# Performance work log

Measured on AMD Instinct MI355X. Metric: run time of the kernel, lower is better.

## Reference

```python
import jax, jax.numpy as jnp
import numpy as np
from jax import lax

V = 50257   # dict_len (vocab)
E = 1024    # w2v_size
H = 1024    # hidden_dim
S = 512     # source length
NSTEPS = 128


def _lstm_cell(h, c, x, W_ih, W_hh, b_ih, b_hh):
    # torch LSTM gate order: i, f, g, o ; W_ih: [4H, in], W_hh: [4H, H]
    gates = x @ W_ih.T + h @ W_hh.T + b_ih + b_hh  # [4H]
    i, f, g, o = jnp.split(gates, 4)
    i = jax.nn.sigmoid(i)
    f = jax.nn.sigmoid(f)
    g = jnp.tanh(g)
    o = jax.nn.sigmoid(o)
    c = f * c + i * g
    h = o * jnp.tanh(c)
    return h, c


def setup_inputs() -> dict:
    key = jax.random.key(0)
    ks = jax.random.split(key, 14)
    s = 0.02
    f32 = jnp.float32
    return {
        "source": jax.random.randint(ks[0], (S,), 0, V),
        "n_steps": NSTEPS,
        "start_token": 1,
        "Wemb_enc": jax.random.normal(ks[1], (V, E), f32) * s,
        "W_ih_e": jax.random.normal(ks[2], (4 * H, E), f32) * s,
        "W_hh_e": jax.random.normal(ks[3], (4 * H, H), f32) * s,
        "b_ih_e": jnp.zeros((4 * H,), f32),
        "b_hh_e": jnp.zeros((4 * H,), f32),
        "Wemb_dec": jax.random.normal(ks[4], (V, E), f32) * s,
        "W_ih_d": jax.random.normal(ks[5], (4 * H, E), f32) * s,
        "W_hh_d": jax.random.normal(ks[6], (4 * H, H), f32) * s,
        "b_ih_d": jnp.zeros((4 * H,), f32),
        "b_hh_d": jnp.zeros((4 * H,), f32),
        "W_out": jax.random.normal(ks[7], (V, H), f32) * s,
        "b_out": jnp.zeros((V,), f32),
    }


def reference(source, n_steps, start_token,
              Wemb_enc, W_ih_e, W_hh_e, b_ih_e, b_hh_e,
              Wemb_dec, W_ih_d, W_hh_d, b_ih_d, b_hh_d,
              W_out, b_out):
    dt = Wemb_enc.dtype

    # ---- encoder: run LSTM over embedded source, keep final (h, c) ----
    xs = Wemb_enc[source]  # [S, E]

    def enc_step(carry, x):
        h, c = carry
        h, c = _lstm_cell(h, c, x, W_ih_e, W_hh_e, b_ih_e, b_hh_e)
        return (h, c), None

    h0 = jnp.zeros((H,), dt)
    c0 = jnp.zeros((H,), dt)
    (h, c), _ = lax.scan(enc_step, (h0, c0), xs)

    def dec_step(carry, _):
        h, c, tok = carry
        x = Wemb_dec[tok]  # [E]
        h, c = _lstm_cell(h, c, x, W_ih_d, W_hh_d, b_ih_d, b_hh_d)
        logits = h @ W_out.T + b_out        # [V]
        probs = jax.nn.softmax(logits)       # module applies Softmax then argmax
        tok = jnp.argmax(probs).astype(jnp.int32)
        return (h, c, tok), (tok, probs)

    tok0 = jnp.asarray(start_token, jnp.int32)
    _, (tokens, probs) = lax.scan(dec_step, (h, c, tok0), None, length=int(n_steps))
    return tokens, probs  # [n_steps] int32, [n_steps, V]
```

## Files before the change

### kernel.cpp

```cpp
#include <hip/hip_runtime.h>
#include <math.h>

#define HDIM  1024
#define VDIM  50257
#define NBLK  256
#define NTHR  1024
#define NWAVE 16

typedef unsigned int uint;

#define WS_GATES   0
#define WS_PSOFT   32768
#define WS_PARGV   33792
#define WS_PARGI   34816
#define WS_PSUM    35840
#define WS_ARRIVE  36864
#define WS_DONE    69632
#define WS_ZOFF    32768
#define WS_ZLEN    40960
#define WS_W8      131072
#define W8_BYTES   ((size_t)VDIM * HDIM)

#if __has_builtin(__builtin_amdgcn_cvt_pk_f32_fp8) && __has_builtin(__builtin_amdgcn_cvt_pk_fp8_f32)
#define FP8_HW 1
#else
#define FP8_HW 0
#endif

__device__ __forceinline__ float dot4(float4 a, float4 b) {
  return a.x * b.x + a.y * b.y + a.z * b.z + a.w * b.w;
}

#if !FP8_HW
__device__ __forceinline__ float fp8d(uint b) {
  uint em = b & 0x7fu;
  float m;
  if (em >= 8u) m = __uint_as_float(((((em >> 3) + 120u) << 23) | ((em & 7u) << 20)));
  else          m = (float)em * 0.001953125f;
  return (b & 0x80u) ? -m : m;
}
__device__ __forceinline__ uint fp8e(float x) {
  uint s = (__float_as_uint(x) >> 24) & 0x80u;
  float ax = fabsf(x);
  uint r;
  if (ax < 0.015625f) {
    r = (uint)rintf(ax * 512.f);
  } else {
    uint b = __float_as_uint(ax);
    b += 0x7ffffu + ((b >> 20) & 1u);
    int  e8 = (int)(b >> 23) - 127 + 7;
    uint m8 = (b >> 20) & 7u;
    if (e8 >= 16 || (e8 == 15 && m8 == 7u)) { e8 = 15; m8 = 6u; }
    r = ((uint)e8 << 3) | m8;
  }
  return r | s;
}
#endif

__device__ __forceinline__ float dot16_fp8(uint4 u, float4 h0, float4 h1,
                                           float4 h2, float4 h3) {
#if FP8_HW
  float s = 0.f;
  { auto a = __builtin_amdgcn_cvt_pk_f32_fp8((int)u.x, false);
    auto b = __builtin_amdgcn_cvt_pk_f32_fp8((int)u.x, true);
    s += a[0] * h0.x + a[1] * h0.y + b[0] * h0.z + b[1] * h0.w; }
  { auto a = __builtin_amdgcn_cvt_pk_f32_fp8((int)u.y, false);
    auto b = __builtin_amdgcn_cvt_pk_f32_fp8((int)u.y, true);
    s += a[0] * h1.x + a[1] * h1.y + b[0] * h1.z + b[1] * h1.w; }
  { auto a = __builtin_amdgcn_cvt_pk_f32_fp8((int)u.z, false);
    auto b = __builtin_amdgcn_cvt_pk_f32_fp8((int)u.z, true);
    s += a[0] * h2.x + a[1] * h2.y + b[0] * h2.z + b[1] * h2.w; }
  { auto a = __builtin_amdgcn_cvt_pk_f32_fp8((int)u.w, false);
    auto b = __builtin_amdgcn_cvt_pk_f32_fp8((int)u.w, true);
    s += a[0] * h3.x + a[1] * h3.y + b[0] * h3.z + b[1] * h3.w; }
  return s;
#else
  float s = 0.f;
  s += fp8d(u.x & 255u) * h0.x + fp8d((u.x >> 8) & 255u) * h0.y +
       fp8d((u.x >> 16) & 255u) * h0.z + fp8d(u.x >> 24) * h0.w;
  s += fp8d(u.y & 255u) * h1.x + fp8d((u.y >> 8) & 255u) * h1.y +
       fp8d((u.y >> 16) & 255u) * h1.z + fp8d(u.y >> 24) * h1.w;
  s += fp8d(u.z & 255u) * h2.x + fp8d((u.z >> 8) & 255u) * h2.y +
       fp8d((u.z >> 16) & 255u) * h2.z + fp8d(u.z >> 24) * h2.w;
  s += fp8d(u.w & 255u) * h3.x + fp8d((u.w >> 8) & 255u) * h3.y +
       fp8d((u.w >> 16) & 255u) * h3.z + fp8d(u.w >> 24) * h3.w;
  return s;
#endif
}

__device__ __forceinline__ float wred64(float v) {
  v += __shfl_xor(v, 32); v += __shfl_xor(v, 16); v += __shfl_xor(v, 8);
  v += __shfl_xor(v, 4);  v += __shfl_xor(v, 2);  v += __shfl_xor(v, 1);
  return v;
}

__device__ __forceinline__ void wmax64(float& v, int& i) {
#pragma unroll
  for (int off = 32; off > 0; off >>= 1) {
    float v2 = __shfl_xor(v, off);
    int   i2 = __shfl_xor(i, off);
    if (v2 > v || (v2 == v && i2 < i)) { v = v2; i = i2; }
  }
}

__device__ __forceinline__ float wvmax64(float v) {
#pragma unroll
  for (int off = 32; off > 0; off >>= 1) v = fmaxf(v, __shfl_xor(v, off));
  return v;
}

__device__ __forceinline__ uint ald(const uint* p) {
  return __hip_atomic_load(p, __ATOMIC_RELAXED, __HIP_MEMORY_SCOPE_AGENT);
}
__device__ __forceinline__ void ast(uint* p, uint v) {
  __hip_atomic_store(p, v, __ATOMIC_RELAXED, __HIP_MEMORY_SCOPE_AGENT);
}
__device__ __forceinline__ float aldf(const float* p) {
  return __hip_atomic_load(p, __ATOMIC_RELAXED, __HIP_MEMORY_SCOPE_AGENT);
}
__device__ __forceinline__ void astf(float* p, float v) {
  __hip_atomic_store(p, v, __ATOMIC_RELAXED, __HIP_MEMORY_SCOPE_AGENT);
}
__device__ __forceinline__ int aldi(const int* p) {
  return __hip_atomic_load(p, __ATOMIC_RELAXED, __HIP_MEMORY_SCOPE_AGENT);
}
__device__ __forceinline__ void asti(int* p, int v) {
  __hip_atomic_store(p, v, __ATOMIC_RELAXED, __HIP_MEMORY_SCOPE_AGENT);
}
__device__ __forceinline__ void fence_vm() {
  asm volatile("s_waitcnt vmcnt(0)" ::: "memory");
}

__device__ __forceinline__ void gbar(uint* arrive, uint* done, uint r) {
  __syncthreads();
  if (blockIdx.x == 0) {
    const int tid = threadIdx.x;
    if (tid >= 1 && tid < NBLK) {
      const uint* slot = arrive + tid * 32;
      while (ald(slot) < r) __builtin_amdgcn_s_sleep(1);
    }
    __syncthreads();
    if (tid < 32) ast(done + tid * 32, r);
  } else {
    if (threadIdx.x == 0) {
      fence_vm();
      ast(arrive + blockIdx.x * 32, r);
      const uint* dl = done + (blockIdx.x >> 3) * 32;
      while (ald(dl) < r) __builtin_amdgcn_s_sleep(1);
    }
    __syncthreads();
  }
}

__global__ void conv8_kernel(const float* __restrict__ W,
                             uint4* __restrict__ o, int n16) {
  int i = blockIdx.x * blockDim.x + threadIdx.x;
  int stride = gridDim.x * blockDim.x;
  const float4* W4 = (const float4*)W;
  for (; i < n16; i += stride) {
    float4 f0 = W4[4 * i], f1 = W4[4 * i + 1], f2 = W4[4 * i + 2], f3 = W4[4 * i + 3];
    uint4 u;
#if FP8_HW
    int p;
    p = __builtin_amdgcn_cvt_pk_fp8_f32(f0.x, f0.y, 0, false);
    p = __builtin_amdgcn_cvt_pk_fp8_f32(f0.z, f0.w, p, true);  u.x = (uint)p;
    p = __builtin_amdgcn_cvt_pk_fp8_f32(f1.x, f1.y, 0, false);
    p = __builtin_amdgcn_cvt_pk_fp8_f32(f1.z, f1.w, p, true);  u.y = (uint)p;
    p = __builtin_amdgcn_cvt_pk_fp8_f32(f2.x, f2.y, 0, false);
    p = __builtin_amdgcn_cvt_pk_fp8_f32(f2.z, f2.w, p, true);  u.z = (uint)p;
    p = __builtin_amdgcn_cvt_pk_fp8_f32(f3.x, f3.y, 0, false);
    p = __builtin_amdgcn_cvt_pk_fp8_f32(f3.z, f3.w, p, true);  u.w = (uint)p;
#else
    u.x = fp8e(f0.x) | (fp8e(f0.y) << 8) | (fp8e(f0.z) << 16) | (fp8e(f0.w) << 24);
    u.y = fp8e(f1.x) | (fp8e(f1.y) << 8) | (fp8e(f1.z) << 16) | (fp8e(f1.w) << 24);
    u.z = fp8e(f2.x) | (fp8e(f2.y) << 8) | (fp8e(f2.z) << 16) | (fp8e(f2.w) << 24);
    u.w = fp8e(f3.x) | (fp8e(f3.y) << 8) | (fp8e(f3.z) << 16) | (fp8e(f3.w) << 24);
#endif
    o[i] = u;
  }
}

template <int Q8>
__global__ void __launch_bounds__(NTHR, 4)
seq2seq_kernel(const int* __restrict__ source, int S,
               const int* __restrict__ n_steps_p, const int* __restrict__ start_tok_p,
               const float* __restrict__ Wemb_enc,
               const float* __restrict__ W_ih_e, const float* __restrict__ W_hh_e,
               const float* __restrict__ b_ih_e, const float* __restrict__ b_hh_e,
               const float* __restrict__ Wemb_dec,
               const float* __restrict__ W_ih_d, const float* __restrict__ W_hh_d,
               const float* __restrict__ b_ih_d, const float* __restrict__ b_hh_d,
               const float* __restrict__ W_out, const float* __restrict__ b_out,
               const uint4* __restrict__ W8,
               float* __restrict__ out,
               float* gates, float* psoft, float* pargv, int* pargi, float* psum,
               uint* arrive, uint* done)
{
  const int tid  = threadIdx.x;
  const int blk  = blockIdx.x;
  const int wave = tid >> 6;
  const int lane = tid & 63;

  __shared__ float4 x4[2][HDIM / 4];
  __shared__ float4 h4[HDIM / 4];
  __shared__ float  hscan[HDIM];
  __shared__ float  c_lds[HDIM];
  __shared__ float  e_lds[200];
  __shared__ float  red_v[NWAVE];
  __shared__ int    red_i[NWAVE];
  __shared__ float  red_s[NWAVE];
  __shared__ float  red_m[NWAVE];
  __shared__ float  red_n[NWAVE];
  __shared__ float  red_v2[NWAVE];
  __shared__ int    red_i2[NWAVE];
  __shared__ int    sh_tok;
  __shared__ float  sh_lmax, sh_S;

  float* h_s = (float*)h4;

  h_s[tid] = 0.f;
  c_lds[tid] = 0.f;

  const int r_e = blk * NWAVE + wave;
  float4 wie[4], whe[4];
  {
    const float4* pie = (const float4*)(W_ih_e + (size_t)r_e * HDIM);
    const float4* phe = (const float4*)(W_hh_e + (size_t)r_e * HDIM);
#pragma unroll
    for (int c = 0; c < 4; ++c) {
      wie[c] = pie[lane + 64 * c];
      whe[c] = phe[lane + 64 * c];
    }
  }
  const float bse = b_ih_e[r_e] + b_hh_e[r_e];

  if (tid < 256)
    x4[0][tid] = ((const float4*)(Wemb_enc + (size_t)source[0] * HDIM))[tid];
  __syncthreads();

  uint rnd = 0;
  int gstep = 0, xb = 0;

  for (int t = 0; t < S; ++t) {
    float4 pf;
    const bool havepf = (t + 1 < S) && (tid < 256);
    if (havepf)
      pf = ((const float4*)(Wemb_enc + (size_t)source[t + 1] * HDIM))[tid];

    float g = bse;
    const float4* xf = (const float4*)&x4[xb][0];
#pragma unroll
    for (int c = 0; c < 4; ++c) {
      g += dot4(wie[c], xf[lane + 64 * c]);
      g += dot4(whe[c], h4[lane + 64 * c]);
    }
    g = wred64(g);
    float* gcur = gates + (gstep & 1) * 4096;
    if (lane == 0) astf(&gcur[r_e], g);

    gbar(arrive, done, ++rnd);

    {
      float ig = aldf(&gcur[tid]),        fg = aldf(&gcur[tid + 1024]);
      float gv = aldf(&gcur[tid + 2048]), og = aldf(&gcur[tid + 3072]);
      float ii = 1.f / (1.f + expf(-ig));
      float ff = 1.f / (1.f + expf(-fg));
      float gt = tanhf(gv);
      float oo = 1.f / (1.f + expf(-og));
      float cc = ff * c_lds[tid] + ii * gt;
      c_lds[tid] = cc;
      h_s[tid]   = oo * tanhf(cc);
    }
    if (havepf) x4[xb ^ 1][tid] = pf;
    __syncthreads();
    xb ^= 1;
    ++gstep;
  }

  const int nsteps = n_steps_p[0];
  const int r_d = blk * NWAVE + wave;
  const float bsd = b_ih_d[r_d] + b_hh_d[r_d];

  float4 wid[4], whd[4];
  {
    const float4* pid = (const float4*)(W_ih_d + (size_t)r_d * HDIM);
    const float4* phd = (const float4*)(W_hh_d + (size_t)r_d * HDIM);
#pragma unroll
    for (int c = 0; c < 4; ++c) {
      wid[c] = pid[lane + 64 * c];
      whd[c] = phd[lane + 64 * c];
    }
  }

  const int start = blk * 196 + (blk < 81 ? blk : 81);
  const int count = 196 + (blk < 81 ? 1 : 0);

  float4 pfx;
  if (tid < 256)
    pfx = ((const float4*)(Wemb_dec + (size_t)start_tok_p[0] * HDIM))[tid];

  for (int t = 0; t < nsteps; ++t) {
    if (tid < 256) x4[0][tid] = pfx;
    __syncthreads();

    {
      const float4* xf = (const float4*)&x4[0][0];
      float g = bsd;
#pragma unroll
      for (int c = 0; c < 4; ++c) {
        g += dot4(wid[c], xf[lane + 64 * c]);
        g += dot4(whd[c], h4[lane + 64 * c]);
      }
      g = wred64(g);
      float* gcur = gates + (gstep & 1) * 4096;
      if (lane == 0) astf(&gcur[r_d], g);
    }
    gbar(arrive, done, ++rnd);
    {
      const float* gcur = gates + (gstep & 1) * 4096;
      float ig = aldf(&gcur[tid]),        fg = aldf(&gcur[tid + 1024]);
      float gv = aldf(&gcur[tid + 2048]), og = aldf(&gcur[tid + 3072]);
      float ii = 1.f / (1.f + expf(-ig));
      float ff = 1.f / (1.f + expf(-fg));
      float gt = tanhf(gv);
      float oo = 1.f / (1.f + expf(-og));
      float cc = ff * c_lds[tid] + ii * gt;
      c_lds[tid] = cc;
      float hv = oo * tanhf(cc);
      h_s[tid] = hv;
      hscan[((((tid >> 2) ^ ((tid >> 5) & 7)) << 2) | (tid & 3))] = hv;
      float h2 = wred64(hv * hv);
      if (lane == 0) red_n[wave] = h2;
    }
    ++gstep;
    __syncthreads();

    if (Q8) {
      const float4* hs4 = (const float4*)hscan;
      const int c0 = 4 * lane;
      float4 h0 = hs4[(c0 + 0) ^ (((c0 + 0) >> 3) & 7)];
      float4 h1 = hs4[(c0 + 1) ^ (((c0 + 1) >> 3) & 7)];
      float4 h2 = hs4[(c0 + 2) ^ (((c0 + 2) >> 3) & 7)];
      float4 h3 = hs4[(c0 + 3) ^ (((c0 + 3) >> 3) & 7)];
      for (int jb = wave * 4; jb < count; jb += NWAVE * 4) {
        int n_ = count - jb;
        const uint4* base = W8 + (((size_t)(start + jb)) << 6) + lane;
        uint4 u0 = base[0];
        uint4 u1 = base[n_ > 1 ? 64 : 0];
        uint4 u2 = base[n_ > 2 ? 128 : 0];
        uint4 u3 = base[n_ > 3 ? 192 : 0];
        float a0 = dot16_fp8(u0, h0, h1, h2, h3);
        float a1 = dot16_fp8(u1, h0, h1, h2, h3);
        float a2 = dot16_fp8(u2, h0, h1, h2, h3);
        float a3 = dot16_fp8(u3, h0, h1, h2, h3);
        a0 = wred64(a0); a1 = wred64(a1); a2 = wred64(a2); a3 = wred64(a3);
        if (lane == 0) {
          e_lds[jb] = a0 + b_out[start + jb];
          if (n_ > 1) e_lds[jb + 1] = a1 + b_out[start + jb + 1];
          if (n_ > 2) e_lds[jb + 2] = a2 + b_out[start + jb + 2];
          if (n_ > 3) e_lds[jb + 3] = a3 + b_out[start + jb + 3];
        }
      }
    } else {
      for (int jb = wave * 4; jb < count; jb += NWAVE * 4) {
        int n_ = count - jb;
        const float4* r0 = (const float4*)(W_out + (size_t)(start + jb) * HDIM);
        const float4* r1 = (const float4*)(W_out + (size_t)(start + jb + (n_ > 1 ? 1 : 0)) * HDIM);
        const float4* r2 = (const float4*)(W_out + (size_t)(start + jb + (n_ > 2 ? 2 : 0)) * HDIM);
        const float4* r3 = (const float4*)(W_out + (size_t)(start + jb + (n_ > 3 ? 3 : 0)) * HDIM);
        float a0 = 0.f, a1 = 0.f, a2 = 0.f, a3 = 0.f;
#pragma unroll
        for (int c = 0; c < 4; ++c) {
          float4 hh = h4[lane + 64 * c];
          a0 += dot4(r0[lane + 64 * c], hh);
          a1 += dot4(r1[lane + 64 * c], hh);
          a2 += dot4(r2[lane + 64 * c], hh);
          a3 += dot4(r3[lane + 64 * c], hh);
        }
        a0 = wred64(a0); a1 = wred64(a1); a2 = wred64(a2); a3 = wred64(a3);
        if (lane == 0) {
          e_lds[jb] = a0 + b_out[start + jb];
          if (n_ > 1) e_lds[jb + 1] = a1 + b_out[start + jb + 1];
          if (n_ > 2) e_lds[jb + 2] = a2 + b_out[start + jb + 2];
          if (n_ > 3) e_lds[jb + 3] = a3 + b_out[start + jb + 3];
        }
      }
    }
    __syncthreads();

    float m_soft; int i_soft;
    {
      float v = -INFINITY; int idx = 0x7fffffff;
      if (tid < count) { v = e_lds[tid]; idx = start + tid; }
      wmax64(v, idx);
      if (lane == 0) { red_v[wave] = v; red_i[wave] = idx; }
    }
    __syncthreads();
    {
      float v = red_v[0]; int idx = red_i[0];
#pragma unroll
      for (int w = 1; w < NWAVE; ++w) {
        float v2 = red_v[w]; int i2 = red_i[w];
        if (v2 > v || (v2 == v && i2 < idx)) { v = v2; idx = i2; }
      }
      m_soft = v; i_soft = idx;
    }

    float pe = (tid < count) ? expf(e_lds[tid] - m_soft) : 0.f;
    {
      float ls = wred64(pe);
      if (lane == 0) red_s[wave] = ls;
    }

    float m_arg = m_soft; int i_arg = i_soft;
    if (Q8) {
      float nrm2 = 0.f;
#pragma unroll
      for (int w = 0; w < NWAVE; ++w) nrm2 += red_n[w];
      float delta = 0.01f * sqrtf(nrm2) + 1e-7f;
      float bv = -INFINITY; int bi = 0x7fffffff;
      for (int j = wave; j < count; j += NWAVE) {
        if (e_lds[j] >= m_soft - delta) {
          const float4* w = (const float4*)(W_out + (size_t)(start + j) * HDIM);
          float a = 0.f;
#pragma unroll
          for (int c = 0; c < 4; ++c) a += dot4(w[lane + 64 * c], h4[lane + 64 * c]);
          a = wred64(a) + b_out[start + j];
          if (a > bv) { bv = a; bi = start + j; }
        }
      }
      if (lane == 0) { red_v2[wave] = bv; red_i2[wave] = bi; }
    }
    __syncthreads();
    float lsum = 0.f;
#pragma unroll
    for (int w = 0; w < NWAVE; ++w) lsum += red_s[w];
    if (Q8) {
      float v = red_v2[0]; int idx = red_i2[0];
#pragma unroll
      for (int w = 1; w < NWAVE; ++w) {
        float v2 = red_v2[w]; int i2 = red_i2[w];
        if (v2 > v || (v2 == v && i2 < idx)) { v = v2; idx = i2; }
      }
      m_arg = v; i_arg = idx;
    }

    if (tid == 0) {
      astf(&psoft[blk], m_soft); astf(&pargv[blk], m_arg);
      asti(&pargi[blk], i_arg);  astf(&psum[blk], lsum);
    }

    ++rnd;
    __syncthreads();
    int tokn; float lmax, Ssum;
    if (blk == 0) {
      if (tid >= 1 && tid < NBLK) {
        const uint* slot = arrive + tid * 32;
        while (ald(slot) < rnd) __builtin_amdgcn_s_sleep(1);
      }
      __syncthreads();
      float v = -INFINITY, m = -INFINITY, mysum = 0.f, myms = 0.f;
      int idx = 0x7fffffff;
      if (tid < NBLK) {
        v     = aldf(&pargv[tid]);
        idx   = aldi(&pargi[tid]);
        m     = aldf(&psoft[tid]);
        mysum = aldf(&psum[tid]);
        myms  = m;
      }
      wmax64(v, idx);
      float mm = wvmax64(m);
      if (lane == 0 && wave < 4) { red_v[wave] = v; red_i[wave] = idx; red_m[wave] = mm; }
      __syncthreads();
      {
        float vv = red_v[0]; int ii2 = red_i[0]; float mmax = red_m[0];
#pragma unroll
        for (int w = 1; w < 4; ++w) {
          float v2 = red_v[w]; int i2 = red_i[w];
          if (v2 > vv || (v2 == vv && i2 < ii2)) { vv = v2; ii2 = i2; }
          mmax = fmaxf(mmax, red_m[w]);
        }
        tokn = ii2; lmax = mmax;
      }
      {
        float s = (tid < NBLK) ? mysum * expf(myms - lmax) : 0.f;
        s = wred64(s);
        if (lane == 0 && wave < 4) red_s[wave] = s;
      }
      __syncthreads();
      Ssum = red_s[0] + red_s[1] + red_s[2] + red_s[3];
      if (tid < 32) {
        uint* dl = done + tid * 32;
        ast(dl + 1, (uint)tokn);
        ast(dl + 2, __float_as_uint(lmax));
        ast(dl + 3, __float_as_uint(Ssum));
        fence_vm();
        ast(dl, rnd);
      }
    } else {
      if (tid == 0) {
        fence_vm();
        ast(arrive + blk * 32, rnd);
        const uint* dl = done + (blk >> 3) * 32;
        while (ald(dl) < rnd) __builtin_amdgcn_s_sleep(1);
        sh_tok  = (int)ald(dl + 1);
        sh_lmax = __uint_as_float(ald(dl + 2));
        sh_S    = __uint_as_float(ald(dl + 3));
      }
      __syncthreads();
      tokn = sh_tok; lmax = sh_lmax; Ssum = sh_S;
    }

    if (tid < 256)
      pfx = ((const float4*)(Wemb_dec + (size_t)tokn * HDIM))[tid];

    float scale = expf(m_soft - lmax) / Ssum;
    if (tid < count)
      out[(size_t)nsteps + (size_t)t * VDIM + start + tid] = pe * scale;
    if (blk == 0 && tid == 0) out[t] = (float)tokn;
  }
}

extern "C" void kernel_launch(void* const* d_in, const int* in_sizes, int n_in,
                              void* d_out, int out_size, void* d_ws, size_t ws_size,
                              hipStream_t stream) {
  const int*   source      = (const int*)d_in[0];
  const int*   n_steps_p   = (const int*)d_in[1];
  const int*   start_tok_p = (const int*)d_in[2];
  const float* Wemb_enc    = (const float*)d_in[3];
  const float* W_ih_e      = (const float*)d_in[4];
  const float* W_hh_e      = (const float*)d_in[5];
  const float* b_ih_e      = (const float*)d_in[6];
  const float* b_hh_e      = (const float*)d_in[7];
  const float* Wemb_dec    = (const float*)d_in[8];
  const float* W_ih_d      = (const float*)d_in[9];
  const float* W_hh_d      = (const float*)d_in[10];
  const float* b_ih_d      = (const float*)d_in[11];
  const float* b_hh_d      = (const float*)d_in[12];
  const float* W_out       = (const float*)d_in[13];
  const float* b_out       = (const float*)d_in[14];
  float*       out         = (float*)d_out;
  int          S           = in_sizes[0];

  char* ws = (char*)d_ws;
  float* gates  = (float*)(ws + WS_GATES);
  float* psoft  = (float*)(ws + WS_PSOFT);
  float* pargv  = (float*)(ws + WS_PARGV);
  int*   pargi  = (int*)  (ws + WS_PARGI);
  float* psum   = (float*)(ws + WS_PSUM);
  uint*  arrive = (uint*) (ws + WS_ARRIVE);
  uint*  done   = (uint*) (ws + WS_DONE);
  uint4* W8     = (uint4*)(ws + WS_W8);

  bool use_q8 = ws_size >= (size_t)WS_W8 + W8_BYTES;

  hipMemsetAsync(ws + WS_ZOFF, 0, WS_ZLEN, stream);

  if (use_q8)
    conv8_kernel<<<2048, 256, 0, stream>>>(W_out, W8, VDIM * HDIM / 16);

  void* args[] = { &source, &S, &n_steps_p, &start_tok_p, &Wemb_enc,
                   &W_ih_e, &W_hh_e, &b_ih_e, &b_hh_e, &Wemb_dec,
                   &W_ih_d, &W_hh_d, &b_ih_d, &b_hh_d, &W_out, &b_out,
                   &W8, &out, &gates, &psoft, &pargv, &pargi, &psum,
                   &arrive, &done };

  void* kfn = use_q8 ? (void*)seq2seq_kernel<1> : (void*)seq2seq_kernel<0>;
  hipLaunchCooperativeKernel(kfn, dim3(NBLK), dim3(NTHR), args, 0, stream);
}
```

Measured before the change: 5.091 ms.

## Split encoder/decoder kernels and cache FP8 output-weight rows in LDS

Splits the fused cooperative kernel into separate encoder and decoder launches, passing the final h/c through workspace. The decoder uses dynamic shared memory to keep up to 128 FP8 W_out rows per block plus b_out resident in LDS, so each step rereads most of its vocab slice from LDS instead of global/L2. The cost is a second cooperative launch, large per-block LDS (about 146 KB) that may limit residency or fail and fall back to a 32-row variant, and extra preload work.

Result: slower. 6.081 ms (+19.5%).

```diff
diff --git a/kernel.cpp b/kernel.cpp
--- a/kernel.cpp
+++ b/kernel.cpp
@@ -14,12 +14,17 @@
 #define WS_PARGV   33792
 #define WS_PARGI   34816
 #define WS_PSUM    35840
-#define WS_ARRIVE  36864
-#define WS_DONE    69632
+#define WS_ARRE    36864
+#define WS_DONE_E  69632
+#define WS_ARRD    73728
+#define WS_DONE_D  106496
+#define WS_HC      110592
 #define WS_ZOFF    32768
-#define WS_ZLEN    40960
+#define WS_ZLEN    77824
 #define WS_W8      131072
 #define W8_BYTES   ((size_t)VDIM * HDIM)
+
+#define DEC_EXTRA  18432
 
 #if __has_builtin(__builtin_amdgcn_cvt_pk_f32_fp8) && __has_builtin(__builtin_amdgcn_cvt_pk_fp8_f32)
 #define FP8_HW 1
@@ -180,21 +185,12 @@
   }
 }
 
-template <int Q8>
 __global__ void __launch_bounds__(NTHR, 4)
-seq2seq_kernel(const int* __restrict__ source, int S,
-               const int* __restrict__ n_steps_p, const int* __restrict__ start_tok_p,
-               const float* __restrict__ Wemb_enc,
-               const float* __restrict__ W_ih_e, const float* __restrict__ W_hh_e,
-               const float* __restrict__ b_ih_e, const float* __restrict__ b_hh_e,
-               const float* __restrict__ Wemb_dec,
-               const float* __restrict__ W_ih_d, const float* __restrict__ W_hh_d,
-               const float* __restrict__ b_ih_d, const float* __restrict__ b_hh_d,
-               const float* __restrict__ W_out, const float* __restrict__ b_out,
-               const uint4* __restrict__ W8,
-               float* __restrict__ out,
-               float* gates, float* psoft, float* pargv, int* pargi, float* psum,
-               uint* arrive, uint* done)
+enc_kernel(const int* __restrict__ source, int S,
+           const float* __restrict__ Wemb_enc,
+           const float* __restrict__ W_ih_e, const float* __restrict__ W_hh_e,
+           const float* __restrict__ b_ih_e, const float* __restrict__ b_hh_e,
+           float* gates, uint* arrive, uint* done, float* hc)
 {
   const int tid  = threadIdx.x;
   const int blk  = blockIdx.x;
@@ -203,21 +199,9 @@
 
   __shared__ float4 x4[2][HDIM / 4];
   __shared__ float4 h4[HDIM / 4];
-  __shared__ float  hscan[HDIM];
   __shared__ float  c_lds[HDIM];
-  __shared__ float  e_lds[200];
-  __shared__ float  red_v[NWAVE];
-  __shared__ int    red_i[NWAVE];
-  __shared__ float  red_s[NWAVE];
-  __shared__ float  red_m[NWAVE];
-  __shared__ float  red_n[NWAVE];
-  __shared__ float  red_v2[NWAVE];
-  __shared__ int    red_i2[NWAVE];
-  __shared__ int    sh_tok;
-  __shared__ float  sh_lmax, sh_S;
 
   float* h_s = (float*)h4;
-
   h_s[tid] = 0.f;
   c_lds[tid] = 0.f;
 
@@ -277,6 +261,50 @@
     ++gstep;
   }
 
+  if (blk == 0 && tid < 256) {
+    ((float4*)hc)[tid]       = ((float4*)h_s)[tid];
+    ((float4*)hc)[256 + tid] = ((float4*)c_lds)[tid];
+  }
+}
+
+template <int LROWS>
+__global__ void __launch_bounds__(NTHR, 4)
+dec_kernel(const int* __restrict__ n_steps_p, const int* __restrict__ start_tok_p,
+           const float* __restrict__ Wemb_dec,
+           const float* __restrict__ W_ih_d, const float* __restrict__ W_hh_d,
+           const float* __restrict__ b_ih_d, const float* __restrict__ b_hh_d,
+           const float* __restrict__ W_out, const float* __restrict__ b_out,
+           const uint4* __restrict__ W8,
+           float* __restrict__ out,
+           float* gates, float* psoft, float* pargv, int* pargi, float* psum,
+           uint* arrive, uint* done, const float* __restrict__ hc)
+{
+  const int tid  = threadIdx.x;
+  const int blk  = blockIdx.x;
+  const int wave = tid >> 6;
+  const int lane = tid & 63;
+
+  extern __shared__ char smem[];
+  uint4* w8l   = (uint4*)smem;
+  char*  base  = smem + (size_t)LROWS * 1024;
+  float4* x4    = (float4*)(base);
+  float4* h4    = (float4*)(base + 4096);
+  float*  hscan = (float*)(base + 8192);
+  float*  c_l   = (float*)(base + 12288);
+  float*  e_l   = (float*)(base + 16384);
+  float*  bo_l  = (float*)(base + 17184);
+  float*  red_v = (float*)(base + 17984);
+  int*    red_i = (int*)  (base + 18048);
+  float*  red_s = (float*)(base + 18112);
+  float*  red_n = (float*)(base + 18176);
+  float*  red_v2= (float*)(base + 18240);
+  int*    red_i2= (int*)  (base + 18304);
+  int*    sh_tok  = (int*)  (base + 18368);
+  float*  sh_lmax = (float*)(base + 18372);
+  float*  sh_S    = (float*)(base + 18376);
+
+  float* h_s = (float*)h4;
+
   const int nsteps = n_steps_p[0];
   const int r_d = blk * NWAVE + wave;
   const float bsd = b_ih_d[r_d] + b_hh_d[r_d];
@@ -295,20 +323,33 @@
   const int start = blk * 196 + (blk < 81 ? blk : 81);
   const int count = 196 + (blk < 81 ? 1 : 0);
 
+  if (tid < 256) {
+    h4[tid]            = ((const float4*)hc)[tid];
+    ((float4*)c_l)[tid]= ((const float4*)hc)[256 + tid];
+  }
+  for (int j = tid; j < count; j += NTHR) bo_l[j] = b_out[start + j];
+  if (LROWS > 0) {
+    const uint4* src = W8 + ((size_t)start << 6);
+    for (int idx = tid; idx < LROWS * 64; idx += NTHR) w8l[idx] = src[idx];
+  }
+
   float4 pfx;
   if (tid < 256)
     pfx = ((const float4*)(Wemb_dec + (size_t)start_tok_p[0] * HDIM))[tid];
+  __syncthreads();
+
+  uint rnd = 0;
+  int gstep = 0;
 
   for (int t = 0; t < nsteps; ++t) {
-    if (tid < 256) x4[0][tid] = pfx;
+    if (tid < 256) x4[tid] = pfx;
     __syncthreads();
 
     {
-      const float4* xf = (const float4*)&x4[0][0];
       float g = bsd;
 #pragma unroll
       for (int c = 0; c < 4; ++c) {
-        g += dot4(wid[c], xf[lane + 64 * c]);
+        g += dot4(wid[c], x4[lane + 64 * c]);
         g += dot4(whd[c], h4[lane + 64 * c]);
       }
       g = wred64(g);
@@ -324,8 +365,8 @@
       float ff = 1.f / (1.f + expf(-fg));
       float gt = tanhf(gv);
       float oo = 1.f / (1.f + expf(-og));
-      float cc = ff * c_lds[tid] + ii * gt;
-      c_lds[tid] = cc;
+      float cc = ff * c_l[tid] + ii * gt;
+      c_l[tid] = cc;
       float hv = oo * tanhf(cc);
       h_s[tid] = hv;
       hscan[((((tid >> 2) ^ ((tid >> 5) & 7)) << 2) | (tid & 3))] = hv;
@@ -335,7 +376,7 @@
     ++gstep;
     __syncthreads();
 
-    if (Q8) {
+    if (LROWS > 0) {
       const float4* hs4 = (const float4*)hscan;
       const int c0 = 4 * lane;
       float4 h0 = hs4[(c0 + 0) ^ (((c0 + 0) >> 3) & 7)];
@@ -344,21 +385,27 @@
       float4 h3 = hs4[(c0 + 3) ^ (((c0 + 3) >> 3) & 7)];
       for (int jb = wave * 4; jb < count; jb += NWAVE * 4) {
         int n_ = count - jb;
-        const uint4* base = W8 + (((size_t)(start + jb)) << 6) + lane;
-        uint4 u0 = base[0];
-        uint4 u1 = base[n_ > 1 ? 64 : 0];
-        uint4 u2 = base[n_ > 2 ? 128 : 0];
-        uint4 u3 = base[n_ > 3 ? 192 : 0];
+        uint4 u0, u1, u2, u3;
+        if (jb + 4 <= LROWS) {
+          const uint4* b0 = w8l + (jb << 6) + lane;
+          u0 = b0[0]; u1 = b0[64]; u2 = b0[128]; u3 = b0[192];
+        } else {
+          const uint4* b0 = W8 + (((size_t)(start + jb)) << 6) + lane;
+          u0 = b0[0];
+          u1 = b0[n_ > 1 ? 64 : 0];
+          u2 = b0[n_ > 2 ? 128 : 0];
+          u3 = b0[n_ > 3 ? 192 : 0];
+        }
         float a0 = dot16_fp8(u0, h0, h1, h2, h3);
         float a1 = dot16_fp8(u1, h0, h1, h2, h3);
         float a2 = dot16_fp8(u2, h0, h1, h2, h3);
         float a3 = dot16_fp8(u3, h0, h1, h2, h3);
         a0 = wred64(a0); a1 = wred64(a1); a2 = wred64(a2); a3 = wred64(a3);
         if (lane == 0) {
-          e_lds[jb] = a0 + b_out[start + jb];
-          if (n_ > 1) e_lds[jb + 1] = a1 + b_out[start + jb + 1];
-          if (n_ > 2) e_lds[jb + 2] = a2 + b_out[start + jb + 2];
-          if (n_ > 3) e_lds[jb + 3] = a3 + b_out[start + jb + 3];
+          e_l[jb] = a0 + bo_l[jb];
+          if (n_ > 1) e_l[jb + 1] = a1 + bo_l[jb + 1];
+          if (n_ > 2) e_l[jb + 2] = a2 + bo_l[jb + 2];
+          if (n_ > 3) e_l[jb + 3] = a3 + bo_l[jb + 3];
         }
       }
     } else {
@@ -379,10 +426,10 @@
         }
         a0 = wred64(a0); a1 = wred64(a1); a2 = wred64(a2); a3 = wred64(a3);
         if (lane == 0) {
-          e_lds[jb] = a0 + b_out[start + jb];
-          if (n_ > 1) e_lds[jb + 1] = a1 + b_out[start + jb + 1];
-          if (n_ > 2) e_lds[jb + 2] = a2 + b_out[start + jb + 2];
-          if (n_ > 3) e_lds[jb + 3] = a3 + b_out[start + jb + 3];
+          e_l[jb] = a0 + bo_l[jb];
+          if (n_ > 1) e_l[jb + 1] = a1 + bo_l[jb + 1];
+          if (n_ > 2) e_l[jb + 2] = a2 + bo_l[jb + 2];
+          if (n_ > 3) e_l[jb + 3] = a3 + bo_l[jb + 3];
         }
       }
     }
@@ -391,7 +438,7 @@
     float m_soft; int i_soft;
     {
       float v = -INFINITY; int idx = 0x7fffffff;
-      if (tid < count) { v = e_lds[tid]; idx = start + tid; }
+      if (tid < count) { v = e_l[tid]; idx = start + tid; }
       wmax64(v, idx);
       if (lane == 0) { red_v[wave] = v; red_i[wave] = idx; }
     }
@@ -406,26 +453,26 @@
       m_soft = v; i_soft = idx;
     }
 
-    float pe = (tid < count) ? expf(e_lds[tid] - m_soft) : 0.f;
+    float pe = (tid < count) ? expf(e_l[tid] - m_soft) : 0.f;
     {
       float ls = wred64(pe);
       if (lane == 0) red_s[wave] = ls;
     }
 
     float m_arg = m_soft; int i_arg = i_soft;
-    if (Q8) {
+    if (LROWS > 0) {
       float nrm2 = 0.f;
 #pragma unroll
       for (int w = 0; w < NWAVE; ++w) nrm2 += red_n[w];
       float delta = 0.01f * sqrtf(nrm2) + 1e-7f;
       float bv = -INFINITY; int bi = 0x7fffffff;
       for (int j = wave; j < count; j += NWAVE) {
-        if (e_lds[j] >= m_soft - delta) {
+        if (e_l[j] >= m_soft - delta) {
           const float4* w = (const float4*)(W_out + (size_t)(start + j) * HDIM);
           float a = 0.f;
 #pragma unroll
           for (int c = 0; c < 4; ++c) a += dot4(w[lane + 64 * c], h4[lane + 64 * c]);
-          a = wred64(a) + b_out[start + j];
+          a = wred64(a) + bo_l[j];
           if (a > bv) { bv = a; bi = start + j; }
         }
       }
@@ -435,7 +482,7 @@
     float lsum = 0.f;
 #pragma unroll
     for (int w = 0; w < NWAVE; ++w) lsum += red_s[w];
-    if (Q8) {
+    if (LROWS > 0) {
       float v = red_v2[0]; int idx = red_i2[0];
 #pragma unroll
       for (int w = 1; w < NWAVE; ++w) {
@@ -470,15 +517,15 @@
       }
       wmax64(v, idx);
       float mm = wvmax64(m);
-      if (lane == 0 && wave < 4) { red_v[wave] = v; red_i[wave] = idx; red_m[wave] = mm; }
+      if (lane == 0 && wave < 4) { red_v[wave] = v; red_i[wave] = idx; red_n[wave] = mm; }
       __syncthreads();
       {
-        float vv = red_v[0]; int ii2 = red_i[0]; float mmax = red_m[0];
+        float vv = red_v[0]; int ii2 = red_i[0]; float mmax = red_n[0];
 #pragma unroll
         for (int w = 1; w < 4; ++w) {
           float v2 = red_v[w]; int i2 = red_i[w];
           if (v2 > vv || (v2 == vv && i2 < ii2)) { vv = v2; ii2 = i2; }
-          mmax = fmaxf(mmax, red_m[w]);
+          mmax = fmaxf(mmax, red_n[w]);
         }
         tokn = ii2; lmax = mmax;
       }
@@ -503,12 +550,12 @@
         ast(arrive + blk * 32, rnd);
         const uint* dl = done + (blk >> 3) * 32;
         while (ald(dl) < rnd) __builtin_amdgcn_s_sleep(1);
-        sh_tok  = (int)ald(dl + 1);
-        sh_lmax = __uint_as_float(ald(dl + 2));
-        sh_S    = __uint_as_float(ald(dl + 3));
+        sh_tok[0]  = (int)ald(dl + 1);
+        sh_lmax[0] = __uint_as_float(ald(dl + 2));
+        sh_S[0]    = __uint_as_float(ald(dl + 3));
       }
       __syncthreads();
-      tokn = sh_tok; lmax = sh_lmax; Ssum = sh_S;
+      tokn = sh_tok[0]; lmax = sh_lmax[0]; Ssum = sh_S[0];
     }
 
     if (tid < 256)
@@ -548,8 +595,11 @@
   float* pargv  = (float*)(ws + WS_PARGV);
   int*   pargi  = (int*)  (ws + WS_PARGI);
   float* psum   = (float*)(ws + WS_PSUM);
-  uint*  arrive = (uint*) (ws + WS_ARRIVE);
-  uint*  done   = (uint*) (ws + WS_DONE);
+  uint*  arrE   = (uint*) (ws + WS_ARRE);
+  uint*  donE   = (uint*) (ws + WS_DONE_E);
+  uint*  arrD   = (uint*) (ws + WS_ARRD);
+  uint*  donD   = (uint*) (ws + WS_DONE_D);
+  float* hc     = (float*)(ws + WS_HC);
   uint4* W8     = (uint4*)(ws + WS_W8);
 
   bool use_q8 = ws_size >= (size_t)WS_W8 + W8_BYTES;
@@ -559,12 +609,34 @@
   if (use_q8)
     conv8_kernel<<<2048, 256, 0, stream>>>(W_out, W8, VDIM * HDIM / 16);
 
-  void* args[] = { &source, &S, &n_steps_p, &start_tok_p, &Wemb_enc,
-                   &W_ih_e, &W_hh_e, &b_ih_e, &b_hh_e, &Wemb_dec,
-                   &W_ih_d, &W_hh_d, &b_ih_d, &b_hh_d, &W_out, &b_out,
-                   &W8, &out, &gates, &psoft, &pargv, &pargi, &psum,
-                   &arrive, &done };
-
-  void* kfn = use_q8 ? (void*)seq2seq_kernel<1> : (void*)seq2seq_kernel<0>;
-  hipLaunchCooperativeKernel(kfn, dim3(NBLK), dim3(NTHR), args, 0, stream);
-}
+  void* eargs[] = { &source, &S, &Wemb_enc, &W_ih_e, &W_hh_e, &b_ih_e, &b_hh_e,
+                    &gates, &arrE, &donE, &hc };
+  hipLaunchCooperativeKernel((void*)enc_kernel, dim3(NBLK), dim3(NTHR),
+                             eargs, 0, stream);
+
+  void* dargs[] = { &n_steps_p, &start_tok_p, &Wemb_dec, &W_ih_d, &W_hh_d,
+                    &b_ih_d, &b_hh_d, &W_out, &b_out, &W8, &out, &gates,
+                    &psoft, &pargv, &pargi, &psum, &arrD, &donD, &hc };
+
+  if (use_q8) {
+    int dyn = 128 * 1024 + DEC_EXTRA;
+    if (hipFuncSetAttribute((const void*)dec_kernel<128>,
+                            hipFuncAttributeMaxDynamicSharedMemorySize,
+                            dyn) == hipSuccess) {
+      hipLaunchCooperativeKernel((void*)dec_kernel<128>, dim3(NBLK), dim3(NTHR),
+                                 dargs, dyn, stream);
+    } else {
+      int dyn2 = 32 * 1024 + DEC_EXTRA;
+      hipFuncSetAttribute((const void*)dec_kernel<32>,
+                          hipFuncAttributeMaxDynamicSharedMemorySize, dyn2);
+      hipLaunchCooperativeKernel((void*)dec_kernel<32>, dim3(NBLK), dim3(NTHR),
+                                 dargs, dyn2, stream);
+    }
+  } else {
+    int dyn0 = DEC_EXTRA;
+    hipFuncSetAttribute((const void*)dec_kernel<0>,
+                        hipFuncAttributeMaxDynamicSharedMemorySize, dyn0);
+    hipLaunchCooperativeKernel((void*)dec_kernel<0>, dim3(NBLK), dim3(NTHR),
+                               dargs, dyn0, stream);
+  }
+}
```
